# Kernel optimization log

Hardware: AMD Instinct MI355X
Metric: run time of the kernel (lower is better)

The kernel has to match this reference:

```python
import jax, jax.numpy as jnp
import numpy as np

B, S, D, H, F, L = 16, 512, 512, 8, 2048, 3  # L layers: 1 in blocks_1 + 2 in blocks_2
DK = D // H
EPS = 1e-5

def setup_inputs():
    key = jax.random.key(0)
    ks = jax.random.split(key, 10)
    sc = 1.0 / np.sqrt(D)
    return dict(
        q_embed_data=jax.random.normal(ks[0], (B, S, D), jnp.float32),
        qa_embed_data=jax.random.normal(ks[1], (B, S, D), jnp.float32),
        Wk=jax.random.normal(ks[2], (L, D, D), jnp.float32) * sc,
        bk=jnp.zeros((L, D), jnp.float32),
        Wv=jax.random.normal(ks[3], (L, D, D), jnp.float32) * sc,
        bv=jnp.zeros((L, D), jnp.float32),
        Wo=jax.random.normal(ks[4], (L, D, D), jnp.float32) * sc,
        bo=jnp.zeros((L, D), jnp.float32),
        gammas=jax.random.normal(ks[5], (L, H, 1, 1), jnp.float32) * 0.5,
        ln1_g=jnp.ones((L, D), jnp.float32),
        ln1_b=jnp.zeros((L, D), jnp.float32),
        W1=jax.random.normal(ks[6], (L, D, F), jnp.float32) * sc,
        b1=jnp.zeros((L, F), jnp.float32),
        W2=jax.random.normal(ks[7], (L, F, D), jnp.float32) * (1.0 / np.sqrt(F)),
        b2=jnp.zeros((L, D), jnp.float32),
        ln2_g=jnp.ones((L, D), jnp.float32),
        ln2_b=jnp.zeros((L, D), jnp.float32),
    )

def _ln(x, g, b):
    m = jnp.mean(x, -1, keepdims=True)
    v = jnp.mean((x - m) ** 2, -1, keepdims=True)
    return (x - m) * jax.lax.rsqrt(v + EPS) * g + b

def _attention(q, k, v, mask, gamma):
    # q,k,v: [B,H,S,DK]; mask: [1,1,S,S] bool; gamma: [H,1,1]
    scores = jnp.einsum('bhid,bhjd->bhij', q, k) / np.sqrt(DK)
    maskf = mask.astype(scores.dtype)
    # first (no-grad in torch) softmax pass for distance decay
    p = jax.nn.softmax(jnp.where(mask, scores, -1e32), axis=-1) * maskf
    distcum = jnp.cumsum(p, axis=-1)
    disttot = jnp.sum(p, axis=-1, keepdims=True)
    idx = jnp.arange(scores.shape[-1])
    pos = jnp.abs(idx[None, :] - idx[:, None]).astype(scores.dtype)[None, None]
    dist = jax.lax.stop_gradient(
        jnp.sqrt(jnp.clip((disttot - distcum) * pos, 0.0, None)))
    g = -jax.nn.softplus(gamma)[None]  # [1,H,1,1]
    total_effect = jnp.clip(jnp.exp(dist * g), 1e-5, 1e5)
    scores = jnp.where(mask, scores * total_effect, -1e32)
    attn = jax.nn.softmax(scores, axis=-1)
    return jnp.einsum('bhij,bhjd->bhid', attn, v)

def _mha(q_in, k_in, v_in, mask, Wk, bk, Wv, bv, Wo, bo, gamma):
    bsz = q_in.shape[0]
    def proj(x, W, b):
        return (x @ W + b).reshape(bsz, -1, H, DK).transpose(0, 2, 1, 3)
    q = proj(q_in, Wk, bk)  # kq_same=True -> q uses k_linear
    k = proj(k_in, Wk, bk)
    v = proj(v_in, Wv, bv)
    o = _attention(q, k, v, mask, gamma)
    o = o.transpose(0, 2, 1, 3).reshape(bsz, -1, D)
    return o @ Wo + bo

def _block(i, mask, query, key, values, apply_pos, P):
    q2 = _mha(query, key, values, mask, P['Wk'][i], P['bk'][i], P['Wv'][i],
              P['bv'][i], P['Wo'][i], P['bo'][i], P['gammas'][i])
    x = _ln(query + q2, P['ln1_g'][i], P['ln1_b'][i])
    if apply_pos:
        h = jax.nn.relu(x @ P['W1'][i] + P['b1'][i]) @ P['W2'][i] + P['b2'][i]
        x = _ln(x + h, P['ln2_g'][i], P['ln2_b'][i])
    return x

def reference(q_embed_data, qa_embed_data, Wk, bk, Wv, bv, Wo, bo, gammas,
              ln1_g, ln1_b, W1, b1, W2, b2, ln2_g, ln2_b):
    P = dict(Wk=Wk, bk=bk, Wv=Wv, bv=bv, Wo=Wo, bo=bo, gammas=gammas,
             ln1_g=ln1_g, ln1_b=ln1_b, W1=W1, b1=b1, W2=W2, b2=b2,
             ln2_g=ln2_g, ln2_b=ln2_b)
    s = q_embed_data.shape[1]
    mask1 = jnp.tril(jnp.ones((s, s), bool))[None, None]        # mask==1: current+past
    mask0 = jnp.tril(jnp.ones((s, s), bool), -1)[None, None]    # mask==0: strictly past
    y = qa_embed_data
    x = q_embed_data
    y = _block(0, mask1, y, y, y, True, P)    # blocks_1: knowledge encoder
    x = _block(1, mask1, x, x, x, False, P)   # blocks_2: question encoder (no FFN)
    x = _block(2, mask0, x, x, y, True, P)    # blocks_2: knowledge retriever
    return x
```

## Files before the change

### kernel.cpp

```cpp
#include <hip/hip_runtime.h>
#include <hip/hip_bf16.h>

#define Bdim 16
#define Sdim 512
#define Ddim 512
#define Hdim 8
#define DKdim 64
#define Fdim 2048
#define Mrows (Bdim * Sdim)

typedef __attribute__((ext_vector_type(8))) short  frag16;
typedef __attribute__((ext_vector_type(4))) float  f32x4;
typedef __attribute__((ext_vector_type(8))) unsigned short ushort8;
typedef __attribute__((ext_vector_type(4))) unsigned short ushort4v;

#if defined(__has_builtin)
#  if __has_builtin(__builtin_amdgcn_exp2f)
#    define EXP2(x) __builtin_amdgcn_exp2f(x)
#  endif
#endif
#ifndef EXP2
#  define EXP2(x) __expf((x) * 0.6931471805599453f)
#endif
#define SC2 0.18033688011112042f

__device__ __forceinline__ unsigned short f2b(float x) {
    union { float f; unsigned int u; } v; v.f = x;
    unsigned int r = (v.u + 0x7FFFu + ((v.u >> 16) & 1u)) >> 16;
    return (unsigned short)r;
}

__global__ __launch_bounds__(256) void gemm_mfma(
    const __hip_bfloat16* __restrict__ A, const __hip_bfloat16* __restrict__ Bt,
    const float* __restrict__ bias, const float* __restrict__ R,
    float* __restrict__ Cf, unsigned short* __restrict__ Cb,
    int M, int N, int K, int do_relu)
{
    __shared__ short As[2][128 * 32];
    __shared__ short Bs[2][128 * 32];

    const int t = threadIdx.x;
    const int lane = t & 63;
    const int wave = t >> 6;

    const int gx = gridDim.x;
    const int nb = gx * gridDim.y;
    const int lid = blockIdx.x + gx * blockIdx.y;
    const int wid = (lid & 7) * (nb >> 3) + (lid >> 3);
    const int bm = (wid / gx) * 128;
    const int bn = (wid % gx) * 128;

    const int wm = (wave >> 1) * 64;
    const int wn = (wave & 1) * 64;

    f32x4 acc[4][4] = {};
    const int lrow = lane >> 2;
    const int lcol = (lane & 3) * 8;

    auto stage = [&](int k0, int buf) {
#pragma unroll
        for (int i = 0; i < 2; ++i) {
            const int chunk = wave * 2 + i;
            const int row = chunk * 16 + lrow;
            const __hip_bfloat16* ga = A + (size_t)(bm + row) * K + k0 + lcol;
            const __hip_bfloat16* gb = Bt + (size_t)(bn + row) * K + k0 + lcol;
            __builtin_amdgcn_global_load_lds(
                (const __attribute__((address_space(1))) unsigned int*)ga,
                (__attribute__((address_space(3))) unsigned int*)(&As[buf][chunk * 512]),
                16, 0, 0);
            __builtin_amdgcn_global_load_lds(
                (const __attribute__((address_space(1))) unsigned int*)gb,
                (__attribute__((address_space(3))) unsigned int*)(&Bs[buf][chunk * 512]),
                16, 0, 0);
        }
    };

    const int fr = lane & 15;
    const int quad = lane >> 4;
    const int nk = K >> 5;

    stage(0, 0);
    __syncthreads();

    for (int it = 0; it < nk; ++it) {
        const int buf = it & 1;
        if (it + 1 < nk) stage((it + 1) << 5, buf ^ 1);
        frag16 af[4], bfr[4];
#pragma unroll
        for (int i = 0; i < 4; ++i) {
            af[i]  = *(const frag16*)(&As[buf][(wm + i * 16 + fr) * 32 + quad * 8]);
            bfr[i] = *(const frag16*)(&Bs[buf][(wn + i * 16 + fr) * 32 + quad * 8]);
        }
#pragma unroll
        for (int mi = 0; mi < 4; ++mi)
#pragma unroll
            for (int ni = 0; ni < 4; ++ni)
                acc[mi][ni] = __builtin_amdgcn_mfma_f32_16x16x32_bf16(
                    af[mi], bfr[ni], acc[mi][ni], 0, 0, 0);
        __syncthreads();
    }

#pragma unroll
    for (int mi = 0; mi < 4; ++mi) {
#pragma unroll
        for (int r = 0; r < 4; ++r) {
            const int m = bm + wm + mi * 16 + quad * 4 + r;
#pragma unroll
            for (int ni = 0; ni < 4; ++ni) {
                const int n = bn + wn + ni * 16 + fr;
                float v = acc[mi][ni][r] + bias[n];
                if (R) v += R[(size_t)m * N + n];
                if (do_relu) v = fmaxf(v, 0.f);
                if (Cf) Cf[(size_t)m * N + n] = v;
                if (Cb) Cb[(size_t)m * N + n] = f2b(v);
            }
        }
    }
}

__global__ __launch_bounds__(256) void gemm_n64(
    const unsigned short* __restrict__ A0, const unsigned short* __restrict__ A1,
    const unsigned short* __restrict__ B0, const unsigned short* __restrict__ B1,
    const float* __restrict__ bias0, const float* __restrict__ bias1,
    const float* __restrict__ R, float* __restrict__ Cf,
    unsigned short* __restrict__ Cb, unsigned short* __restrict__ CbT,
    int K)
{
    const int NN = 512;
    __shared__ short As[2][128 * 64];
    __shared__ short Bs[2][64 * 64];

    const int trans = blockIdx.z;
    const unsigned short* A  = trans ? A1 : A0;
    const unsigned short* Bt = trans ? B1 : B0;
    const float* bias        = trans ? bias1 : bias0;

    const int t = threadIdx.x;
    const int lane = t & 63;
    const int wave = t >> 6;

    const int lid = blockIdx.x + 8 * blockIdx.y;
    const int wid = (lid & 7) * 64 + (lid >> 3);
    const int bm = (wid >> 3) * 128;
    const int bn = (wid & 7) * 64;

    const int wm = (wave >> 1) * 64;
    const int wn = (wave & 1) * 32;

    f32x4 acc[4][2] = {};

    const int srcslot = (((lane & 7) ^ (lane >> 3)) << 3);
    const int rsub = lane >> 3;

    auto stage = [&](int k0, int buf) {
#pragma unroll
        for (int i = 0; i < 4; ++i) {
            const int row = i * 32 + wave * 8 + rsub;
            const unsigned short* ga = A + (size_t)(bm + row) * K + k0 + srcslot;
            __builtin_amdgcn_global_load_lds(
                (const __attribute__((address_space(1))) unsigned int*)ga,
                (__attribute__((address_space(3))) unsigned int*)(&As[buf][(i * 256 + wave * 64) * 8]),
                16, 0, 0);
        }
#pragma unroll
        for (int i = 0; i < 2; ++i) {
            const int row = i * 32 + wave * 8 + rsub;
            const unsigned short* gb = Bt + (size_t)(bn + row) * K + k0 + srcslot;
            __builtin_amdgcn_global_load_lds(
                (const __attribute__((address_space(1))) unsigned int*)gb,
                (__attribute__((address_space(3))) unsigned int*)(&Bs[buf][(i * 256 + wave * 64) * 8]),
                16, 0, 0);
        }
    };

    const int fr = lane & 15;
    const int quad = lane >> 4;
    const int sw = (fr & 7) << 3;
    const int nk = K >> 6;

    stage(0, 0);
    __syncthreads();

    for (int it = 0; it < nk; ++it) {
        const int buf = it & 1;
        if (it + 1 < nk) stage((it + 1) << 6, buf ^ 1);
        frag16 af[2][4], bfr[2][2];
#pragma unroll
        for (int ks = 0; ks < 2; ++ks) {
            const int col = (ks * 32 + quad * 8) ^ sw;
#pragma unroll
            for (int i = 0; i < 4; ++i)
                af[ks][i] = *(const frag16*)(&As[buf][(wm + i * 16 + fr) * 64 + col]);
#pragma unroll
            for (int i = 0; i < 2; ++i)
                bfr[ks][i] = *(const frag16*)(&Bs[buf][(wn + i * 16 + fr) * 64 + col]);
        }
#pragma unroll
        for (int ks = 0; ks < 2; ++ks)
#pragma unroll
            for (int mi = 0; mi < 4; ++mi)
#pragma unroll
                for (int ni = 0; ni < 2; ++ni)
                    acc[mi][ni] = __builtin_amdgcn_mfma_f32_16x16x32_bf16(
                        af[ks][mi], bfr[ks][ni], acc[mi][ni], 0, 0, 0);
        __syncthreads();
    }

    if (trans) {
#pragma unroll
        for (int mi = 0; mi < 4; ++mi)
#pragma unroll
            for (int ni = 0; ni < 2; ++ni) {
                const int m = bm + wm + mi * 16 + quad * 4;
                const int n = bn + wn + ni * 16 + fr;
                ushort4v o;
#pragma unroll
                for (int r = 0; r < 4; ++r) o[r] = f2b(acc[mi][ni][r] + bias[n]);
                const int bb = m >> 9, s = m & 511;
                const int hh = n >> 6, dd = n & 63;
                *(ushort4v*)(CbT + (((size_t)((bb * Hdim + hh) * DKdim + dd)) << 9) + s) = o;
            }
        return;
    }

#pragma unroll
    for (int mi = 0; mi < 4; ++mi) {
#pragma unroll
        for (int r = 0; r < 4; ++r) {
            const int m = bm + wm + mi * 16 + quad * 4 + r;
#pragma unroll
            for (int ni = 0; ni < 2; ++ni) {
                const int n = bn + wn + ni * 16 + fr;
                float v = acc[mi][ni][r] + bias[n];
                if (R) v += R[(size_t)m * NN + n];
                if (Cf) Cf[(size_t)m * NN + n] = v;
                if (Cb) Cb[(size_t)m * NN + n] = f2b(v);
            }
        }
    }
}

__global__ __launch_bounds__(256) void gemm_ffn2(
    const unsigned short* __restrict__ A, const unsigned short* __restrict__ Bt,
    const float* __restrict__ bias, const float* __restrict__ R,
    float* __restrict__ C0, float* __restrict__ C1)
{
    const int K = 2048, KH = 1024;
    __shared__ short As[2][128 * 64];
    __shared__ short Bs[2][64 * 64];

    const int z = blockIdx.z;
    const int kbase = z * KH;

    const int t = threadIdx.x;
    const int lane = t & 63;
    const int wave = t >> 6;

    const int lid = blockIdx.x + 8 * blockIdx.y;
    const int wid = (lid & 7) * 64 + (lid >> 3);
    const int bm = (wid >> 3) * 128;
    const int bn = (wid & 7) * 64;

    const int wm = (wave >> 1) * 64;
    const int wn = (wave & 1) * 32;

    f32x4 acc[4][2] = {};
    const int srcslot = (((lane & 7) ^ (lane >> 3)) << 3);
    const int rsub = lane >> 3;

    auto stage = [&](int k0, int buf) {
#pragma unroll
        for (int i = 0; i < 4; ++i) {
            const int row = i * 32 + wave * 8 + rsub;
            const unsigned short* ga = A + (size_t)(bm + row) * K + k0 + srcslot;
            __builtin_amdgcn_global_load_lds(
                (const __attribute__((address_space(1))) unsigned int*)ga,
                (__attribute__((address_space(3))) unsigned int*)(&As[buf][(i * 256 + wave * 64) * 8]),
                16, 0, 0);
        }
#pragma unroll
        for (int i = 0; i < 2; ++i) {
            const int row = i * 32 + wave * 8 + rsub;
            const unsigned short* gb = Bt + (size_t)(bn + row) * K + k0 + srcslot;
            __builtin_amdgcn_global_load_lds(
                (const __attribute__((address_space(1))) unsigned int*)gb,
                (__attribute__((address_space(3))) unsigned int*)(&Bs[buf][(i * 256 + wave * 64) * 8]),
                16, 0, 0);
        }
    };

    const int fr = lane & 15;
    const int quad = lane >> 4;
    const int sw = (fr & 7) << 3;
    const int nk = KH >> 6;

    stage(kbase, 0);
    __syncthreads();

    for (int it = 0; it < nk; ++it) {
        const int buf = it & 1;
        if (it + 1 < nk) stage(kbase + ((it + 1) << 6), buf ^ 1);
        frag16 af[2][4], bfr[2][2];
#pragma unroll
        for (int ks = 0; ks < 2; ++ks) {
            const int col = (ks * 32 + quad * 8) ^ sw;
#pragma unroll
            for (int i = 0; i < 4; ++i)
                af[ks][i] = *(const frag16*)(&As[buf][(wm + i * 16 + fr) * 64 + col]);
#pragma unroll
            for (int i = 0; i < 2; ++i)
                bfr[ks][i] = *(const frag16*)(&Bs[buf][(wn + i * 16 + fr) * 64 + col]);
        }
#pragma unroll
        for (int ks = 0; ks < 2; ++ks)
#pragma unroll
            for (int mi = 0; mi < 4; ++mi)
#pragma unroll
                for (int ni = 0; ni < 2; ++ni)
                    acc[mi][ni] = __builtin_amdgcn_mfma_f32_16x16x32_bf16(
                        af[ks][mi], bfr[ks][ni], acc[mi][ni], 0, 0, 0);
        __syncthreads();
    }

#pragma unroll
    for (int mi = 0; mi < 4; ++mi) {
#pragma unroll
        for (int r = 0; r < 4; ++r) {
            const int m = bm + wm + mi * 16 + quad * 4 + r;
#pragma unroll
            for (int ni = 0; ni < 2; ++ni) {
                const int n = bn + wn + ni * 16 + fr;
                if (z == 0)
                    C0[(size_t)m * 512 + n] = acc[mi][ni][r] + bias[n] + R[(size_t)m * 512 + n];
                else
                    C1[(size_t)m * 512 + n] = acc[mi][ni][r];
            }
        }
    }
}

__global__ __launch_bounds__(256) void gemm_kv4(
    const unsigned short* __restrict__ Ya, const unsigned short* __restrict__ Xa,
    const unsigned short* __restrict__ BtK0, const unsigned short* __restrict__ BtV0,
    const unsigned short* __restrict__ BtK1, const unsigned short* __restrict__ BtV1,
    const float* __restrict__ bk0, const float* __restrict__ bv0,
    const float* __restrict__ bk1, const float* __restrict__ bv1,
    unsigned short* __restrict__ K0, unsigned short* __restrict__ V0t,
    unsigned short* __restrict__ K1, unsigned short* __restrict__ V1t)
{
    const int K = 512;
    __shared__ short As[2][128 * 64];
    __shared__ short Bs[2][64 * 64];

    const int z = blockIdx.z;
    const unsigned short* A  = (z < 2) ? Ya : Xa;
    const unsigned short* Bt = (z == 0) ? BtK0 : (z == 1) ? BtV0 : (z == 2) ? BtK1 : BtV1;
    const float* bias        = (z == 0) ? bk0 : (z == 1) ? bv0 : (z == 2) ? bk1 : bv1;
    const int trans = z & 1;

    const int t = threadIdx.x;
    const int lane = t & 63;
    const int wave = t >> 6;

    const int lid = blockIdx.x + 8 * blockIdx.y;
    const int wid = (lid & 7) * 64 + (lid >> 3);
    const int bm = (wid >> 3) * 128;
    const int bn = (wid & 7) * 64;

    const int wm = (wave >> 1) * 64;
    const int wn = (wave & 1) * 32;

    f32x4 acc[4][2] = {};
    const int srcslot = (((lane & 7) ^ (lane >> 3)) << 3);
    const int rsub = lane >> 3;

    auto stage = [&](int k0, int buf) {
#pragma unroll
        for (int i = 0; i < 4; ++i) {
            const int row = i * 32 + wave * 8 + rsub;
            const unsigned short* ga = A + (size_t)(bm + row) * K + k0 + srcslot;
            __builtin_amdgcn_global_load_lds(
                (const __attribute__((address_space(1))) unsigned int*)ga,
                (__attribute__((address_space(3))) unsigned int*)(&As[buf][(i * 256 + wave * 64) * 8]),
                16, 0, 0);
        }
#pragma unroll
        for (int i = 0; i < 2; ++i) {
            const int row = i * 32 + wave * 8 + rsub;
            const unsigned short* gb = Bt + (size_t)(bn + row) * K + k0 + srcslot;
            __builtin_amdgcn_global_load_lds(
                (const __attribute__((address_space(1))) unsigned int*)gb,
                (__attribute__((address_space(3))) unsigned int*)(&Bs[buf][(i * 256 + wave * 64) * 8]),
                16, 0, 0);
        }
    };

    const int fr = lane & 15;
    const int quad = lane >> 4;
    const int sw = (fr & 7) << 3;
    const int nk = K >> 6;

    stage(0, 0);
    __syncthreads();

    for (int it = 0; it < nk; ++it) {
        const int buf = it & 1;
        if (it + 1 < nk) stage((it + 1) << 6, buf ^ 1);
        frag16 af[2][4], bfr[2][2];
#pragma unroll
        for (int ks = 0; ks < 2; ++ks) {
            const int col = (ks * 32 + quad * 8) ^ sw;
#pragma unroll
            for (int i = 0; i < 4; ++i)
                af[ks][i] = *(const frag16*)(&As[buf][(wm + i * 16 + fr) * 64 + col]);
#pragma unroll
            for (int i = 0; i < 2; ++i)
                bfr[ks][i] = *(const frag16*)(&Bs[buf][(wn + i * 16 + fr) * 64 + col]);
        }
#pragma unroll
        for (int ks = 0; ks < 2; ++ks)
#pragma unroll
            for (int mi = 0; mi < 4; ++mi)
#pragma unroll
                for (int ni = 0; ni < 2; ++ni)
                    acc[mi][ni] = __builtin_amdgcn_mfma_f32_16x16x32_bf16(
                        af[ks][mi], bfr[ks][ni], acc[mi][ni], 0, 0, 0);
        __syncthreads();
    }

    if (trans) {
        unsigned short* CbT = (z == 1) ? V0t : V1t;
#pragma unroll
        for (int mi = 0; mi < 4; ++mi)
#pragma unroll
            for (int ni = 0; ni < 2; ++ni) {
                const int m = bm + wm + mi * 16 + quad * 4;
                const int n = bn + wn + ni * 16 + fr;
                ushort4v o;
#pragma unroll
                for (int r = 0; r < 4; ++r) o[r] = f2b(acc[mi][ni][r] + bias[n]);
                const int bb = m >> 9, s = m & 511;
                const int hh = n >> 6, dd = n & 63;
                *(ushort4v*)(CbT + (((size_t)((bb * Hdim + hh) * DKdim + dd)) << 9) + s) = o;
            }
    } else {
        unsigned short* Cb = (z == 0) ? K0 : K1;
#pragma unroll
        for (int mi = 0; mi < 4; ++mi)
#pragma unroll
            for (int r = 0; r < 4; ++r) {
                const int m = bm + wm + mi * 16 + quad * 4 + r;
#pragma unroll
                for (int ni = 0; ni < 2; ++ni) {
                    const int n = bn + wn + ni * 16 + fr;
                    Cb[(size_t)m * 512 + n] = f2b(acc[mi][ni][r] + bias[n]);
                }
            }
    }
}

__global__ __launch_bounds__(256) void gemm_o2(
    const unsigned short* __restrict__ A0, const unsigned short* __restrict__ A1,
    const unsigned short* __restrict__ B0, const unsigned short* __restrict__ B1,
    const float* __restrict__ bias0, const float* __restrict__ bias1,
    const float* __restrict__ R0, const float* __restrict__ R1,
    float* __restrict__ C0, float* __restrict__ C1)
{
    const int K = 512;
    __shared__ short As[2][128 * 64];
    __shared__ short Bs[2][64 * 64];

    const int z = blockIdx.z;
    const unsigned short* A  = z ? A1 : A0;
    const unsigned short* Bt = z ? B1 : B0;
    const float* bias        = z ? bias1 : bias0;
    const float* R           = z ? R1 : R0;
    float* Cf                = z ? C1 : C0;

    const int t = threadIdx.x;
    const int lane = t & 63;
    const int wave = t >> 6;

    const int lid = blockIdx.x + 8 * blockIdx.y;
    const int wid = (lid & 7) * 64 + (lid >> 3);
    const int bm = (wid >> 3) * 128;
    const int bn = (wid & 7) * 64;

    const int wm = (wave >> 1) * 64;
    const int wn = (wave & 1) * 32;

    f32x4 acc[4][2] = {};
    const int srcslot = (((lane & 7) ^ (lane >> 3)) << 3);
    const int rsub = lane >> 3;

    auto stage = [&](int k0, int buf) {
#pragma unroll
        for (int i = 0; i < 4; ++i) {
            const int row = i * 32 + wave * 8 + rsub;
            const unsigned short* ga = A + (size_t)(bm + row) * K + k0 + srcslot;
            __builtin_amdgcn_global_load_lds(
                (const __attribute__((address_space(1))) unsigned int*)ga,
                (__attribute__((address_space(3))) unsigned int*)(&As[buf][(i * 256 + wave * 64) * 8]),
                16, 0, 0);
        }
#pragma unroll
        for (int i = 0; i < 2; ++i) {
            const int row = i * 32 + wave * 8 + rsub;
            const unsigned short* gb = Bt + (size_t)(bn + row) * K + k0 + srcslot;
            __builtin_amdgcn_global_load_lds(
                (const __attribute__((address_space(1))) unsigned int*)gb,
                (__attribute__((address_space(3))) unsigned int*)(&Bs[buf][(i * 256 + wave * 64) * 8]),
                16, 0, 0);
        }
    };

    const int fr = lane & 15;
    const int quad = lane >> 4;
    const int sw = (fr & 7) << 3;
    const int nk = K >> 6;

    stage(0, 0);
    __syncthreads();

    for (int it = 0; it < nk; ++it) {
        const int buf = it & 1;
        if (it + 1 < nk) stage((it + 1) << 6, buf ^ 1);
        frag16 af[2][4], bfr[2][2];
#pragma unroll
        for (int ks = 0; ks < 2; ++ks) {
            const int col = (ks * 32 + quad * 8) ^ sw;
#pragma unroll
            for (int i = 0; i < 4; ++i)
                af[ks][i] = *(const frag16*)(&As[buf][(wm + i * 16 + fr) * 64 + col]);
#pragma unroll
            for (int i = 0; i < 2; ++i)
                bfr[ks][i] = *(const frag16*)(&Bs[buf][(wn + i * 16 + fr) * 64 + col]);
        }
#pragma unroll
        for (int ks = 0; ks < 2; ++ks)
#pragma unroll
            for (int mi = 0; mi < 4; ++mi)
#pragma unroll
                for (int ni = 0; ni < 2; ++ni)
                    acc[mi][ni] = __builtin_amdgcn_mfma_f32_16x16x32_bf16(
                        af[ks][mi], bfr[ks][ni], acc[mi][ni], 0, 0, 0);
        __syncthreads();
    }

#pragma unroll
    for (int mi = 0; mi < 4; ++mi) {
#pragma unroll
        for (int r = 0; r < 4; ++r) {
            const int m = bm + wm + mi * 16 + quad * 4 + r;
#pragma unroll
            for (int ni = 0; ni < 2; ++ni) {
                const int n = bn + wn + ni * 16 + fr;
                Cf[(size_t)m * 512 + n] = acc[mi][ni][r] + bias[n] + R[(size_t)m * 512 + n];
            }
        }
    }
}

__global__ __launch_bounds__(256) void conv_b2(
    const float* __restrict__ X0, unsigned short* __restrict__ Y0,
    const float* __restrict__ X1, unsigned short* __restrict__ Y1,
    int halfBlocks)
{
    const int bid = blockIdx.x;
    const float* X = (bid < halfBlocks) ? X0 : X1;
    unsigned short* Y = (bid < halfBlocks) ? Y0 : Y1;
    const int lb = (bid < halfBlocks) ? bid : bid - halfBlocks;
    const size_t i = ((size_t)lb * 256 + threadIdx.x) * 8;
    float4 a = *(const float4*)(X + i);
    float4 b = *(const float4*)(X + i + 4);
    ushort8 o;
    o[0] = f2b(a.x); o[1] = f2b(a.y); o[2] = f2b(a.z); o[3] = f2b(a.w);
    o[4] = f2b(b.x); o[5] = f2b(b.y); o[6] = f2b(b.z); o[7] = f2b(b.w);
    *(ushort8*)(Y + i) = o;
}

__global__ __launch_bounds__(256) void wtrans_all(
    const float* __restrict__ Wk, const float* __restrict__ Wv,
    const float* __restrict__ Wo, const float* __restrict__ W1,
    const float* __restrict__ W2, unsigned short* __restrict__ dst)
{
    const int bid = blockIdx.x;
    const float* src; unsigned short* d; int K, N, tk, tn;
    if (bid < 576) {
        const int mat = bid >> 6, tile = bid & 63;
        const int l = mat / 3, wch = mat % 3;
        const float* W = (wch == 0) ? Wk : (wch == 1) ? Wv : Wo;
        src = W + (size_t)l * 262144;
        d = dst + (size_t)mat * 262144;
        K = 512; N = 512; tn = tile & 7; tk = tile >> 3;
    } else if (bid < 1088) {
        const int idx = bid - 576, l2 = idx >> 8, tile = idx & 255;
        src = W1 + (size_t)(l2 * 2) * (512 * 2048);
        d = dst + 9 * 262144 + (size_t)l2 * (512 * 2048);
        K = 512; N = 2048; tn = tile & 31; tk = tile >> 5;
    } else {
        const int idx = bid - 1088, l2 = idx >> 8, tile = idx & 255;
        src = W2 + (size_t)(l2 * 2) * (2048 * 512);
        d = dst + 9 * 262144 + 2 * (512 * 2048) + (size_t)l2 * (2048 * 512);
        K = 2048; N = 512; tn = tile & 7; tk = tile >> 3;
    }
    const int n0 = tn * 64, k0 = tk * 64;
    __shared__ float T[64][65];
    const int t = threadIdx.x;
    const int kl = t >> 4, n4 = (t & 15) << 2;
#pragma unroll
    for (int it = 0; it < 4; ++it) {
        const int k = kl + it * 16;
        float4 v = *(const float4*)(src + (size_t)(k0 + k) * N + n0 + n4);
        T[n4 + 0][k] = v.x; T[n4 + 1][k] = v.y;
        T[n4 + 2][k] = v.z; T[n4 + 3][k] = v.w;
    }
    __syncthreads();
    const int nl = t >> 3, k8 = (t & 7) << 3;
#pragma unroll
    for (int it = 0; it < 2; ++it) {
        const int n = nl + it * 32;
        ushort8 o;
#pragma unroll
        for (int c = 0; c < 8; ++c) o[c] = f2b(T[n][k8 + c]);
        *(ushort8*)(d + (size_t)(n0 + n) * K + k0 + k8) = o;
    }
}

__global__ __launch_bounds__(256, 8) void attn_flash8(
    const unsigned short* __restrict__ Kb0, const unsigned short* __restrict__ Vt0,
    const unsigned short* __restrict__ Kb1, const unsigned short* __restrict__ Vt1,
    const float* __restrict__ gam,
    unsigned short* __restrict__ Ob0, unsigned short* __restrict__ Ob1,
    int mask_type, int dual)
{
    __shared__ float CTw[16 * 33];
    __shared__ unsigned short Pst[4][16 * 36];
    __shared__ float S1s[4][16];
    __shared__ float S2s[4][16];
    __shared__ float OaccA[16 * 66];
    __shared__ float OaccB[16 * 66];

    int bh, layer;
    if (dual) { layer = blockIdx.x & 1; bh = blockIdx.x >> 1; }
    else      { layer = 0;              bh = blockIdx.x; }
    const unsigned short* Kb = layer ? Kb1 : Kb0;
    const unsigned short* Vt = layer ? Vt1 : Vt0;
    unsigned short* Ob       = layer ? Ob1 : Ob0;
    const float* g           = gam + layer * Hdim;

    const int h = bh & 7, b = bh >> 3;
    const int rk = blockIdx.y;
    const int tile = mask_type ? (31 - rk) : (rk == 0 ? 0 : 32 - rk);

    const int t = threadIdx.x, lane = t & 63, w = t >> 6;
    const int quad = lane >> 4, fr = lane & 15;
    const int q0 = tile * 16;
    const int iRow = q0 + fr;

    const unsigned short* kbase = Kb + (size_t)b * Sdim * Ddim + h * DKdim;
    const unsigned short* vtb = Vt + (size_t)(b * Hdim + h) * DKdim * Sdim;
    const float gneg2 = -log1pf(__expf(g[h])) * 1.4426950408889634f;

    frag16 aq0 = *(const frag16*)(kbase + (size_t)(q0 + fr) * Ddim + quad * 8);
    frag16 aq1 = *(const frag16*)(kbase + (size_t)(q0 + fr) * Ddim + 32 + quad * 8);

    float psum = 0.f;
    for (int jn = w; jn <= tile; jn += 4) {
        frag16 k0 = *(const frag16*)(kbase + (size_t)(jn * 16 + fr) * Ddim + quad * 8);
        frag16 k1 = *(const frag16*)(kbase + (size_t)(jn * 16 + fr) * Ddim + 32 + quad * 8);
        f32x4 z = {0.f, 0.f, 0.f, 0.f};
        z = __builtin_amdgcn_mfma_f32_16x16x32_bf16(k0, aq0, z, 0, 0, 0);
        z = __builtin_amdgcn_mfma_f32_16x16x32_bf16(k1, aq1, z, 0, 0, 0);
        float tq = 0.f;
        if (jn < tile) {
#pragma unroll
            for (int r = 0; r < 4; ++r) tq += EXP2(z[r] * SC2);
        } else {
#pragma unroll
            for (int r = 0; r < 4; ++r) {
                const bool valid = mask_type ? (quad * 4 + r <= fr)
                                             : (quad * 4 + r < fr);
                tq += valid ? EXP2(z[r] * SC2) : 0.f;
            }
        }
        psum += tq;
        float tt = tq;
        tt += __shfl_xor(tt, 16);
        tt += __shfl_xor(tt, 32);
        if (quad == 0) CTw[fr * 33 + jn] = tt;
    }
    {
        float s1 = psum;
        s1 += __shfl_xor(s1, 16);
        s1 += __shfl_xor(s1, 32);
        if (lane < 16) S1s[w][lane] = s1;
    }
    __syncthreads();

    if (w == 0 && lane < 16) {
        float run = 0.f;
        for (int jn = tile; jn >= 0; --jn) {
            const float tv = CTw[lane * 33 + jn];
            CTw[lane * 33 + jn] = run;
            run += tv;
        }
    }
    __syncthreads();

    const float rsum1 = 1.f / (S1s[0][fr] + S1s[1][fr] + S1s[2][fr] + S1s[3][fr]);
    unsigned short* Pw = Pst[w];
    const bool fm_blk = (mask_type == 0) && (tile == 0);
    const bool fmrow = fm_blk && (fr == 0);
    const int umax = fm_blk ? (Sdim / 32 - 1) : (tile >> 1);
    float sum2p = 0.f;
    f32x4 oacc[4] = {};

    for (int u = umax - w; u >= 0; u -= 4) {
#pragma unroll
        for (int half = 0; half < 2; ++half) {
            const int jn = 2 * u + half;
            uint2 pku;
            if (jn > tile) {
                const unsigned int pv = fmrow ? 0x3F803F80u : 0u;
                pku.x = pv; pku.y = pv;
                sum2p += fmrow ? 4.f : 0.f;
            } else {
                frag16 k0 = *(const frag16*)(kbase + (size_t)(jn * 16 + fr) * Ddim + quad * 8);
                frag16 k1 = *(const frag16*)(kbase + (size_t)(jn * 16 + fr) * Ddim + 32 + quad * 8);
                f32x4 z = {0.f, 0.f, 0.f, 0.f};
                z = __builtin_amdgcn_mfma_f32_16x16x32_bf16(k0, aq0, z, 0, 0, 0);
                z = __builtin_amdgcn_mfma_f32_16x16x32_bf16(k1, aq1, z, 0, 0, 0);
                const bool full = (jn < tile);
                float s2r[4], lsuf[4];
                float tq = 0.f;
#pragma unroll
                for (int r = 3; r >= 0; --r) {
                    lsuf[r] = tq;
                    s2r[r] = z[r] * SC2;
                    float e1 = EXP2(s2r[r]);
                    if (!full) {
                        const bool valid = mask_type ? (quad * 4 + r <= fr)
                                                     : (quad * 4 + r < fr);
                        e1 = valid ? e1 : 0.f;
                    }
                    tq += e1;
                }
                float incl = tq;
                {
                    float u1 = __shfl_down(incl, 16);
                    incl += (quad < 3) ? u1 : 0.f;
                    float u2 = __shfl_down(incl, 32);
                    incl += (quad < 2) ? u2 : 0.f;
                }
                const float base = CTw[fr * 33 + jn] + (incl - tq);
                const float pos0 = (float)(iRow - (jn * 16 + quad * 4));
                float e2v[4];
#pragma unroll
                for (int r = 0; r < 4; ++r) {
                    const float ratio = (base + lsuf[r]) * rsum1;
                    const float arg = ratio * fabsf(pos0 - (float)r);
                    const float te = fmaxf(EXP2(gneg2 * sqrtf(arg)), 1e-5f);
                    float e2 = EXP2(s2r[r] * te);
                    if (!full) {
                        const bool valid = mask_type ? (quad * 4 + r <= fr)
                                                     : (quad * 4 + r < fr);
                        e2 = valid ? e2 : (fmrow ? 1.f : 0.f);
                    }
                    sum2p += e2;
                    e2v[r] = e2;
                }
                union { __hip_bfloat162 hh; unsigned int u; } c0, c1;
                c0.hh = __float22bfloat162_rn(make_float2(e2v[0], e2v[1]));
                c1.hh = __float22bfloat162_rn(make_float2(e2v[2], e2v[3]));
                pku.x = c0.u; pku.y = c1.u;
            }
            *(uint2*)(Pw + fr * 36 + half * 16 + quad * 4) = pku;
        }
        frag16 pf = *(const frag16*)(Pw + fr * 36 + quad * 8);
        const int jb = u * 32;
#pragma unroll
        for (int dt = 0; dt < 4; ++dt) {
            frag16 vf = *(const frag16*)(vtb + (size_t)(dt * 16 + fr) * Sdim + jb + quad * 8);
            oacc[dt] = __builtin_amdgcn_mfma_f32_16x16x32_bf16(pf, vf, oacc[dt], 0, 0, 0);
        }
    }

    {
        float s2 = sum2p;
        s2 += __shfl_xor(s2, 16);
        s2 += __shfl_xor(s2, 32);
        if (lane < 16) S2s[w][lane] = s2;
    }
    if (w == 1) {
#pragma unroll
        for (int dt = 0; dt < 4; ++dt)
#pragma unroll
            for (int r = 0; r < 4; ++r)
                OaccA[(quad * 4 + r) * 66 + dt * 16 + fr] = oacc[dt][r];
    }
    if (w == 3) {
#pragma unroll
        for (int dt = 0; dt < 4; ++dt)
#pragma unroll
            for (int r = 0; r < 4; ++r)
                OaccB[(quad * 4 + r) * 66 + dt * 16 + fr] = oacc[dt][r];
    }
    __syncthreads();
    if (w == 0) {
#pragma unroll
        for (int dt = 0; dt < 4; ++dt)
#pragma unroll
            for (int r = 0; r < 4; ++r)
                oacc[dt][r] += OaccA[(quad * 4 + r) * 66 + dt * 16 + fr];
    }
    if (w == 2) {
#pragma unroll
        for (int dt = 0; dt < 4; ++dt)
#pragma unroll
            for (int r = 0; r < 4; ++r)
                oacc[dt][r] += OaccB[(quad * 4 + r) * 66 + dt * 16 + fr];
    }
    __syncthreads();
    if (w == 2) {
#pragma unroll
        for (int dt = 0; dt < 4; ++dt)
#pragma unroll
            for (int r = 0; r < 4; ++r)
                OaccA[(quad * 4 + r) * 66 + dt * 16 + fr] = oacc[dt][r];
    }
    __syncthreads();

    if (w == 0) {
        const float rs2 = 1.f / (S2s[0][fr] + S2s[1][fr] + S2s[2][fr] + S2s[3][fr]);
        float rs2q[4];
#pragma unroll
        for (int r = 0; r < 4; ++r) rs2q[r] = __shfl(rs2, quad * 4 + r);

        unsigned short* obase = Ob + ((size_t)(b * Sdim + q0)) * Ddim + h * DKdim;
#pragma unroll
        for (int dt = 0; dt < 4; ++dt)
#pragma unroll
            for (int r = 0; r < 4; ++r) {
                const float v = oacc[dt][r] + OaccA[(quad * 4 + r) * 66 + dt * 16 + fr];
                obase[(size_t)(quad * 4 + r) * Ddim + dt * 16 + fr] = f2b(v * rs2q[r]);
            }
    }
}

__device__ __forceinline__ void ln_row_wave(
    const float* __restrict__ X, const float* __restrict__ P,
    const float* __restrict__ g, const float* __restrict__ bta,
    float* __restrict__ Y, unsigned short* __restrict__ Yb,
    int row, int lane)
{
    const size_t base = (size_t)row * Ddim + lane * 8;
    float4 a = *(const float4*)(X + base);
    float4 b = *(const float4*)(X + base + 4);
    if (P) {
        float4 pa = *(const float4*)(P + base);
        float4 pb = *(const float4*)(P + base + 4);
        a.x += pa.x; a.y += pa.y; a.z += pa.z; a.w += pa.w;
        b.x += pb.x; b.y += pb.y; b.z += pb.z; b.w += pb.w;
    }
    float s  = a.x + a.y + a.z + a.w + b.x + b.y + b.z + b.w;
    float s2 = a.x * a.x + a.y * a.y + a.z * a.z + a.w * a.w
             + b.x * b.x + b.y * b.y + b.z * b.z + b.w * b.w;
#pragma unroll
    for (int off = 1; off < 64; off <<= 1) {
        s  += __shfl_xor(s, off);
        s2 += __shfl_xor(s2, off);
    }
    const float mean = s * (1.f / Ddim);
    const float var = s2 * (1.f / Ddim) - mean * mean;
    const float rs = rsqrtf(var + 1e-5f);
    float4 ga = *(const float4*)(g + lane * 8);
    float4 gb = *(const float4*)(g + lane * 8 + 4);
    float4 ba = *(const float4*)(bta + lane * 8);
    float4 bb = *(const float4*)(bta + lane * 8 + 4);
    float y[8];
    y[0] = (a.x - mean) * rs * ga.x + ba.x;
    y[1] = (a.y - mean) * rs * ga.y + ba.y;
    y[2] = (a.z - mean) * rs * ga.z + ba.z;
    y[3] = (a.w - mean) * rs * ga.w + ba.w;
    y[4] = (b.x - mean) * rs * gb.x + bb.x;
    y[5] = (b.y - mean) * rs * gb.y + bb.y;
    y[6] = (b.z - mean) * rs * gb.z + bb.z;
    y[7] = (b.w - mean) * rs * gb.w + bb.w;
    if (Y) {
        *(float4*)(Y + base)     = make_float4(y[0], y[1], y[2], y[3]);
        *(float4*)(Y + base + 4) = make_float4(y[4], y[5], y[6], y[7]);
    }
    if (Yb) {
        ushort8 o;
#pragma unroll
        for (int c = 0; c < 8; ++c) o[c] = f2b(y[c]);
        *(ushort8*)(Yb + base) = o;
    }
}

__global__ __launch_bounds__(256) void ln_w1(
    const float* __restrict__ X, const float* __restrict__ P,
    const float* __restrict__ g, const float* __restrict__ bta,
    float* __restrict__ Y, unsigned short* __restrict__ Yb)
{
    const int row = blockIdx.x * 4 + (threadIdx.x >> 6);
    ln_row_wave(X, P, g, bta, Y, Yb, row, threadIdx.x & 63);
}

__global__ __launch_bounds__(256) void ln_w2(
    const float* __restrict__ Xa, const float* __restrict__ ga,
    const float* __restrict__ ba, float* __restrict__ Ya,
    unsigned short* __restrict__ Yba,
    const float* __restrict__ Xb, const float* __restrict__ gb,
    const float* __restrict__ bb, float* __restrict__ Yb2,
    unsigned short* __restrict__ Ybb)
{
    const int row = blockIdx.x * 4 + (threadIdx.x >> 6);
    if (row < Mrows)
        ln_row_wave(Xa, nullptr, ga, ba, Ya, Yba, row, threadIdx.x & 63);
    else
        ln_row_wave(Xb, nullptr, gb, bb, Yb2, Ybb, row - Mrows, threadIdx.x & 63);
}

extern "C" void kernel_launch(void* const* d_in, const int* in_sizes, int n_in,
                              void* d_out, int out_size, void* d_ws, size_t ws_size,
                              hipStream_t stream)
{
    const float* x0     = (const float*)d_in[0];
    const float* y0     = (const float*)d_in[1];
    const float* Wk     = (const float*)d_in[2];
    const float* bk     = (const float*)d_in[3];
    const float* Wv     = (const float*)d_in[4];
    const float* bv     = (const float*)d_in[5];
    const float* Wo     = (const float*)d_in[6];
    const float* bo     = (const float*)d_in[7];
    const float* gammas = (const float*)d_in[8];
    const float* ln1g   = (const float*)d_in[9];
    const float* ln1b   = (const float*)d_in[10];
    const float* W1     = (const float*)d_in[11];
    const float* b1     = (const float*)d_in[12];
    const float* W2     = (const float*)d_in[13];
    const float* b2     = (const float*)d_in[14];
    const float* ln2g   = (const float*)d_in[15];
    const float* ln2b   = (const float*)d_in[16];

    const size_t NBSD = (size_t)Mrows * Ddim;
    float* ws = (float*)d_ws;
    float* T1   = ws;
    float* X1   = T1 + NBSD;
    float* Xbuf = X1 + NBSD;
    unsigned short* Kbf = (unsigned short*)(Xbuf + NBSD);
    unsigned short* Vt  = Kbf + NBSD;
    unsigned short* AOb = Vt + NBSD;
    unsigned short* Abf = AOb + NBSD;
    unsigned short* Xbf = Abf + NBSD;
    unsigned short* Ybf = Xbf + NBSD;
    unsigned short* Hbb = Ybf + NBSD;
    unsigned short* WtAll = Hbb + (size_t)Mrows * Fdim;

    unsigned short* Xb_in = Hbb;
    unsigned short* AOb1  = Hbb + NBSD;
    unsigned short* Yb_in = Hbb + 2 * NBSD;
    unsigned short* Kbf1  = Abf;
    unsigned short* Vt1   = Ybf;
    float* T1b = (float*)d_out;
    float* P1  = (float*)AOb;

    auto WtK = [&](int l) { return WtAll + (size_t)(l * 3 + 0) * 262144; };
    auto WtV = [&](int l) { return WtAll + (size_t)(l * 3 + 1) * 262144; };
    auto WtO = [&](int l) { return WtAll + (size_t)(l * 3 + 2) * 262144; };
    auto Wt1 = [&](int l) { return WtAll + 9 * 262144 + (size_t)(l >> 1) * (512 * 2048); };
    auto Wt2 = [&](int l) { return WtAll + 9 * 262144 + 2 * (512 * 2048) + (size_t)(l >> 1) * (2048 * 512); };

    const int convBlocks = (int)(NBSD / 2048);

    wtrans_all<<<1600, 256, 0, stream>>>(Wk, Wv, Wo, W1, W2, WtAll);
    conv_b2<<<2 * convBlocks, 256, 0, stream>>>(y0, Yb_in, x0, Xb_in, convBlocks);
    gemm_kv4<<<dim3(8, 64, 4), 256, 0, stream>>>(
        Yb_in, Xb_in, WtK(0), WtV(0), WtK(1), WtV(1),
        bk, bv, bk + Ddim, bv + Ddim,
        Kbf, Vt, Kbf1, Vt1);
    attn_flash8<<<dim3(2 * Bdim * Hdim, Sdim / 16, 1), 256, 0, stream>>>(
        Kbf, Vt, Kbf1, Vt1, gammas, AOb, AOb1, 1, 1);
    gemm_o2<<<dim3(8, 64, 2), 256, 0, stream>>>(
        AOb, AOb1, WtO(0), WtO(1), bo, bo + Ddim, y0, x0, T1, T1b);
    ln_w2<<<2 * Mrows / 4, 256, 0, stream>>>(
        T1, ln1g, ln1b, X1, Abf,
        T1b, ln1g + Ddim, ln1b + Ddim, Xbuf, Xbf);
    gemm_mfma<<<dim3(Fdim / 128, Mrows / 128), 256, 0, stream>>>(
        (const __hip_bfloat16*)Abf, (const __hip_bfloat16*)Wt1(0),
        b1, nullptr, nullptr, Hbb, Mrows, Fdim, Ddim, 1);
    gemm_ffn2<<<dim3(8, 64, 2), 256, 0, stream>>>(
        Hbb, Wt2(0), b2, X1, T1, P1);
    ln_w1<<<Mrows / 4, 256, 0, stream>>>(T1, P1, ln2g, ln2b, nullptr, Ybf);

    const int l = 2;
    gemm_n64<<<dim3(8, 64, 2), 256, 0, stream>>>(
        Xbf, Ybf, WtK(l), WtV(l), bk + l * Ddim, bv + l * Ddim,
        nullptr, nullptr, Kbf, Vt, Ddim);
    attn_flash8<<<dim3(Bdim * Hdim, Sdim / 16, 1), 256, 0, stream>>>(
        Kbf, Vt, Kbf, Vt, gammas + (size_t)l * Hdim, AOb, AOb, 0, 0);
    gemm_n64<<<dim3(8, 64, 1), 256, 0, stream>>>(
        AOb, AOb, WtO(l), WtO(l), bo + l * Ddim, bo + l * Ddim,
        Xbuf, T1, nullptr, nullptr, Ddim);
    ln_w1<<<Mrows / 4, 256, 0, stream>>>(T1, nullptr,
        ln1g + (size_t)l * Ddim, ln1b + (size_t)l * Ddim, X1, Abf);
    gemm_mfma<<<dim3(Fdim / 128, Mrows / 128), 256, 0, stream>>>(
        (const __hip_bfloat16*)Abf, (const __hip_bfloat16*)Wt1(l),
        b1 + (size_t)l * Fdim, nullptr, nullptr, Hbb, Mrows, Fdim, Ddim, 1);
    gemm_ffn2<<<dim3(8, 64, 2), 256, 0, stream>>>(
        Hbb, Wt2(l), b2 + (size_t)l * Ddim, X1, T1, P1);
    ln_w1<<<Mrows / 4, 256, 0, stream>>>(T1, P1,
        ln2g + (size_t)l * Ddim, ln2b + (size_t)l * Ddim, (float*)d_out, nullptr);
}
```

Before: 562.4 us.

## Split-K the output projections and use 32-bit offsets in attention

Generalizes the FFN2 split-K kernel to take K as a parameter and applies it to the layer-2 output projection. gemm_o2 is now split in half along K over four z-slices, with the second half's partial sums folded in by the LayerNorm kernels. The goal is more blocks per launch for these short-K GEMMs, at the cost of extra fp32 partial-buffer traffic. The attention kernel switches to precomputed 32-bit unsigned offsets and computes sqrt as x*rsqrt to trim address and ALU work. gemm_o2's partial buffers alias X1 and Xbuf, which are read and written in place by ln_w2.

```diff
diff --git a/kernel.cpp b/kernel.cpp
--- a/kernel.cpp
+++ b/kernel.cpp
@@ -240,17 +240,17 @@
     }
 }
 
-__global__ __launch_bounds__(256) void gemm_ffn2(
+__global__ __launch_bounds__(256) void gemm_splitk(
     const unsigned short* __restrict__ A, const unsigned short* __restrict__ Bt,
     const float* __restrict__ bias, const float* __restrict__ R,
-    float* __restrict__ C0, float* __restrict__ C1)
-{
-    const int K = 2048, KH = 1024;
+    float* __restrict__ C0, float* __restrict__ C1,
+    int K, int KH)
+{
     __shared__ short As[2][128 * 64];
     __shared__ short Bs[2][64 * 64];
 
     const int z = blockIdx.z;
-    const int kbase = z * KH;
+    const int kb0 = z * KH;
 
     const int t = threadIdx.x;
     const int lane = t & 63;
@@ -294,12 +294,12 @@
     const int sw = (fr & 7) << 3;
     const int nk = KH >> 6;
 
-    stage(kbase, 0);
+    stage(kb0, 0);
     __syncthreads();
 
     for (int it = 0; it < nk; ++it) {
         const int buf = it & 1;
-        if (it + 1 < nk) stage(kbase + ((it + 1) << 6), buf ^ 1);
+        if (it + 1 < nk) stage(kb0 + ((it + 1) << 6), buf ^ 1);
         frag16 af[2][4], bfr[2][2];
 #pragma unroll
         for (int ks = 0; ks < 2; ++ks) {
@@ -464,18 +464,20 @@
     const unsigned short* __restrict__ B0, const unsigned short* __restrict__ B1,
     const float* __restrict__ bias0, const float* __restrict__ bias1,
     const float* __restrict__ R0, const float* __restrict__ R1,
-    float* __restrict__ C0, float* __restrict__ C1)
-{
-    const int K = 512;
+    float* __restrict__ C0, float* __restrict__ C1,
+    float* __restrict__ P0, float* __restrict__ P1)
+{
+    const int K = 512, KH = 256;
     __shared__ short As[2][128 * 64];
     __shared__ short Bs[2][64 * 64];
 
-    const int z = blockIdx.z;
-    const unsigned short* A  = z ? A1 : A0;
-    const unsigned short* Bt = z ? B1 : B0;
-    const float* bias        = z ? bias1 : bias0;
-    const float* R           = z ? R1 : R0;
-    float* Cf                = z ? C1 : C0;
+    const int zl = blockIdx.z >> 1, kh = blockIdx.z & 1;
+    const unsigned short* A  = zl ? A1 : A0;
+    const unsigned short* Bt = zl ? B1 : B0;
+    const float* bias        = zl ? bias1 : bias0;
+    const float* R           = zl ? R1 : R0;
+    float* Cf                = kh ? (zl ? P1 : P0) : (zl ? C1 : C0);
+    const int kb0 = kh * KH;
 
     const int t = threadIdx.x;
     const int lane = t & 63;
@@ -517,14 +519,14 @@
     const int fr = lane & 15;
     const int quad = lane >> 4;
     const int sw = (fr & 7) << 3;
-    const int nk = K >> 6;
-
-    stage(0, 0);
+    const int nk = KH >> 6;
+
+    stage(kb0, 0);
     __syncthreads();
 
     for (int it = 0; it < nk; ++it) {
         const int buf = it & 1;
-        if (it + 1 < nk) stage((it + 1) << 6, buf ^ 1);
+        if (it + 1 < nk) stage(kb0 + ((it + 1) << 6), buf ^ 1);
         frag16 af[2][4], bfr[2][2];
 #pragma unroll
         for (int ks = 0; ks < 2; ++ks) {
@@ -555,7 +557,9 @@
 #pragma unroll
             for (int ni = 0; ni < 2; ++ni) {
                 const int n = bn + wn + ni * 16 + fr;
-                Cf[(size_t)m * 512 + n] = acc[mi][ni][r] + bias[n] + R[(size_t)m * 512 + n];
+                float v = acc[mi][ni][r];
+                if (kh == 0) v += bias[n] + R[(size_t)m * 512 + n];
+                Cf[(size_t)m * 512 + n] = v;
             }
         }
     }
@@ -627,7 +631,7 @@
     }
 }
 
-__global__ __launch_bounds__(256, 8) void attn_flash8(
+__global__ __launch_bounds__(256, 8) void attn_flash9(
     const unsigned short* __restrict__ Kb0, const unsigned short* __restrict__ Vt0,
     const unsigned short* __restrict__ Kb1, const unsigned short* __restrict__ Vt1,
     const float* __restrict__ gam,
@@ -662,33 +666,39 @@
     const unsigned short* vtb = Vt + (size_t)(b * Hdim + h) * DKdim * Sdim;
     const float gneg2 = -log1pf(__expf(g[h])) * 1.4426950408889634f;
 
-    frag16 aq0 = *(const frag16*)(kbase + (size_t)(q0 + fr) * Ddim + quad * 8);
-    frag16 aq1 = *(const frag16*)(kbase + (size_t)(q0 + fr) * Ddim + 32 + quad * 8);
+    const unsigned lane_off = ((unsigned)fr << 9) + (unsigned)quad * 8;
+    const unsigned kvstep = 16u * Ddim;
+
+    frag16 aq0 = *(const frag16*)(kbase + ((unsigned)q0 << 9) + lane_off);
+    frag16 aq1 = *(const frag16*)(kbase + ((unsigned)q0 << 9) + lane_off + 32);
 
     float psum = 0.f;
-    for (int jn = w; jn <= tile; jn += 4) {
-        frag16 k0 = *(const frag16*)(kbase + (size_t)(jn * 16 + fr) * Ddim + quad * 8);
-        frag16 k1 = *(const frag16*)(kbase + (size_t)(jn * 16 + fr) * Ddim + 32 + quad * 8);
-        f32x4 z = {0.f, 0.f, 0.f, 0.f};
-        z = __builtin_amdgcn_mfma_f32_16x16x32_bf16(k0, aq0, z, 0, 0, 0);
-        z = __builtin_amdgcn_mfma_f32_16x16x32_bf16(k1, aq1, z, 0, 0, 0);
-        float tq = 0.f;
-        if (jn < tile) {
-#pragma unroll
-            for (int r = 0; r < 4; ++r) tq += EXP2(z[r] * SC2);
-        } else {
-#pragma unroll
-            for (int r = 0; r < 4; ++r) {
-                const bool valid = mask_type ? (quad * 4 + r <= fr)
-                                             : (quad * 4 + r < fr);
-                tq += valid ? EXP2(z[r] * SC2) : 0.f;
+    {
+        unsigned ko = (unsigned)w * kvstep + lane_off;
+        for (int jn = w; jn <= tile; jn += 4, ko += 4 * kvstep) {
+            frag16 k0 = *(const frag16*)(kbase + ko);
+            frag16 k1 = *(const frag16*)(kbase + ko + 32);
+            f32x4 z = {0.f, 0.f, 0.f, 0.f};
+            z = __builtin_amdgcn_mfma_f32_16x16x32_bf16(k0, aq0, z, 0, 0, 0);
+            z = __builtin_amdgcn_mfma_f32_16x16x32_bf16(k1, aq1, z, 0, 0, 0);
+            float tq = 0.f;
+            if (jn < tile) {
+#pragma unroll
+                for (int r = 0; r < 4; ++r) tq += EXP2(z[r] * SC2);
+            } else {
+#pragma unroll
+                for (int r = 0; r < 4; ++r) {
+                    const bool valid = mask_type ? (quad * 4 + r <= fr)
+                                                 : (quad * 4 + r < fr);
+                    tq += valid ? EXP2(z[r] * SC2) : 0.f;
+                }
             }
-        }
-        psum += tq;
-        float tt = tq;
-        tt += __shfl_xor(tt, 16);
-        tt += __shfl_xor(tt, 32);
-        if (quad == 0) CTw[fr * 33 + jn] = tt;
+            psum += tq;
+            float tt = tq;
+            tt += __shfl_xor(tt, 16);
+            tt += __shfl_xor(tt, 32);
+            if (quad == 0) CTw[fr * 33 + jn] = tt;
+        }
     }
     {
         float s1 = psum;
@@ -717,6 +727,7 @@
     f32x4 oacc[4] = {};
 
     for (int u = umax - w; u >= 0; u -= 4) {
+        const unsigned ko2 = ((unsigned)u << 14) + lane_off;
 #pragma unroll
         for (int half = 0; half < 2; ++half) {
             const int jn = 2 * u + half;
@@ -726,8 +737,9 @@
                 pku.x = pv; pku.y = pv;
                 sum2p += fmrow ? 4.f : 0.f;
             } else {
-                frag16 k0 = *(const frag16*)(kbase + (size_t)(jn * 16 + fr) * Ddim + quad * 8);
-                frag16 k1 = *(const frag16*)(kbase + (size_t)(jn * 16 + fr) * Ddim + 32 + quad * 8);
+                const unsigned koh = ko2 + (unsigned)half * kvstep;
+                frag16 k0 = *(const frag16*)(kbase + koh);
+                frag16 k1 = *(const frag16*)(kbase + koh + 32);
                 f32x4 z = {0.f, 0.f, 0.f, 0.f};
                 z = __builtin_amdgcn_mfma_f32_16x16x32_bf16(k0, aq0, z, 0, 0, 0);
                 z = __builtin_amdgcn_mfma_f32_16x16x32_bf16(k1, aq1, z, 0, 0, 0);
@@ -760,7 +772,8 @@
                 for (int r = 0; r < 4; ++r) {
                     const float ratio = (base + lsuf[r]) * rsum1;
                     const float arg = ratio * fabsf(pos0 - (float)r);
-                    const float te = fmaxf(EXP2(gneg2 * sqrtf(arg)), 1e-5f);
+                    const float sq = arg * rsqrtf(fmaxf(arg, 1e-30f));
+                    const float te = fmaxf(EXP2(gneg2 * sq), 1e-5f);
                     float e2 = EXP2(s2r[r] * te);
                     if (!full) {
                         const bool valid = mask_type ? (quad * 4 + r <= fr)
@@ -778,10 +791,10 @@
             *(uint2*)(Pw + fr * 36 + half * 16 + quad * 4) = pku;
         }
         frag16 pf = *(const frag16*)(Pw + fr * 36 + quad * 8);
-        const int jb = u * 32;
+        const unsigned vo = lane_off + ((unsigned)u << 5);
 #pragma unroll
         for (int dt = 0; dt < 4; ++dt) {
-            frag16 vf = *(const frag16*)(vtb + (size_t)(dt * 16 + fr) * Sdim + jb + quad * 8);
+            frag16 vf = *(const frag16*)(vtb + vo + (unsigned)dt * 8192u);
             oacc[dt] = __builtin_amdgcn_mfma_f32_16x16x32_bf16(pf, vf, oacc[dt], 0, 0, 0);
         }
     }
@@ -909,18 +922,18 @@
 }
 
 __global__ __launch_bounds__(256) void ln_w2(
-    const float* __restrict__ Xa, const float* __restrict__ ga,
-    const float* __restrict__ ba, float* __restrict__ Ya,
-    unsigned short* __restrict__ Yba,
-    const float* __restrict__ Xb, const float* __restrict__ gb,
-    const float* __restrict__ bb, float* __restrict__ Yb2,
-    unsigned short* __restrict__ Ybb)
+    const float* __restrict__ Xa, const float* __restrict__ Pa,
+    const float* __restrict__ ga, const float* __restrict__ ba,
+    float* __restrict__ Ya, unsigned short* __restrict__ Yba,
+    const float* __restrict__ Xb, const float* __restrict__ Pb,
+    const float* __restrict__ gb, const float* __restrict__ bb,
+    float* __restrict__ Yb2, unsigned short* __restrict__ Ybb)
 {
     const int row = blockIdx.x * 4 + (threadIdx.x >> 6);
     if (row < Mrows)
-        ln_row_wave(Xa, nullptr, ga, ba, Ya, Yba, row, threadIdx.x & 63);
+        ln_row_wave(Xa, Pa, ga, ba, Ya, Yba, row, threadIdx.x & 63);
     else
-        ln_row_wave(Xb, nullptr, gb, bb, Yb2, Ybb, row - Mrows, threadIdx.x & 63);
+        ln_row_wave(Xb, Pb, gb, bb, Yb2, Ybb, row - Mrows, threadIdx.x & 63);
 }
 
 extern "C" void kernel_launch(void* const* d_in, const int* in_sizes, int n_in,
@@ -966,6 +979,7 @@
     unsigned short* Vt1   = Ybf;
     float* T1b = (float*)d_out;
     float* P1  = (float*)AOb;
+    float* PO2 = (float*)Hbb;
 
     auto WtK = [&](int l) { return WtAll + (size_t)(l * 3 + 0) * 262144; };
     auto WtV = [&](int l) { return WtAll + (size_t)(l * 3 + 1) * 262144; };
@@ -981,36 +995,36 @@
         Yb_in, Xb_in, WtK(0), WtV(0), WtK(1), WtV(1),
         bk, bv, bk + Ddim, bv + Ddim,
         Kbf, Vt, Kbf1, Vt1);
-    attn_flash8<<<dim3(2 * Bdim * Hdim, Sdim / 16, 1), 256, 0, stream>>>(
+    attn_flash9<<<dim3(2 * Bdim * Hdim, Sdim / 16, 1), 256, 0, stream>>>(
         Kbf, Vt, Kbf1, Vt1, gammas, AOb, AOb1, 1, 1);
-    gemm_o2<<<dim3(8, 64, 2), 256, 0, stream>>>(
-        AOb, AOb1, WtO(0), WtO(1), bo, bo + Ddim, y0, x0, T1, T1b);
+    gemm_o2<<<dim3(8, 64, 4), 256, 0, stream>>>(
+        AOb, AOb1, WtO(0), WtO(1), bo, bo + Ddim, y0, x0,
+        T1, T1b, X1 , Xbuf );
     ln_w2<<<2 * Mrows / 4, 256, 0, stream>>>(
-        T1, ln1g, ln1b, X1, Abf,
-        T1b, ln1g + Ddim, ln1b + Ddim, Xbuf, Xbf);
+        T1, X1, ln1g, ln1b, X1, Abf,
+        T1b, Xbuf, ln1g + Ddim, ln1b + Ddim, Xbuf, Xbf);
     gemm_mfma<<<dim3(Fdim / 128, Mrows / 128), 256, 0, stream>>>(
         (const __hip_bfloat16*)Abf, (const __hip_bfloat16*)Wt1(0),
         b1, nullptr, nullptr, Hbb, Mrows, Fdim, Ddim, 1);
-    gemm_ffn2<<<dim3(8, 64, 2), 256, 0, stream>>>(
-        Hbb, Wt2(0), b2, X1, T1, P1);
+    gemm_splitk<<<dim3(8, 64, 2), 256, 0, stream>>>(
+        Hbb, Wt2(0), b2, X1, T1, P1, 2048, 1024);
     ln_w1<<<Mrows / 4, 256, 0, stream>>>(T1, P1, ln2g, ln2b, nullptr, Ybf);
 
     const int l = 2;
     gemm_n64<<<dim3(8, 64, 2), 256, 0, stream>>>(
         Xbf, Ybf, WtK(l), WtV(l), bk + l * Ddim, bv + l * Ddim,
         nullptr, nullptr, Kbf, Vt, Ddim);
-    attn_flash8<<<dim3(Bdim * Hdim, Sdim / 16, 1), 256, 0, stream>>>(
+    attn_flash9<<<dim3(Bdim * Hdim, Sdim / 16, 1), 256, 0, stream>>>(
         Kbf, Vt, Kbf, Vt, gammas + (size_t)l * Hdim, AOb, AOb, 0, 0);
-    gemm_n64<<<dim3(8, 64, 1), 256, 0, stream>>>(
-        AOb, AOb, WtO(l), WtO(l), bo + l * Ddim, bo + l * Ddim,
-        Xbuf, T1, nullptr, nullptr, Ddim);
-    ln_w1<<<Mrows / 4, 256, 0, stream>>>(T1, nullptr,
+    gemm_splitk<<<dim3(8, 64, 2), 256, 0, stream>>>(
+        AOb, WtO(l), bo + l * Ddim, Xbuf, T1, PO2, 512, 256);
+    ln_w1<<<Mrows / 4, 256, 0, stream>>>(T1, PO2,
         ln1g + (size_t)l * Ddim, ln1b + (size_t)l * Ddim, X1, Abf);
     gemm_mfma<<<dim3(Fdim / 128, Mrows / 128), 256, 0, stream>>>(
         (const __hip_bfloat16*)Abf, (const __hip_bfloat16*)Wt1(l),
         b1 + (size_t)l * Fdim, nullptr, nullptr, Hbb, Mrows, Fdim, Ddim, 1);
-    gemm_ffn2<<<dim3(8, 64, 2), 256, 0, stream>>>(
-        Hbb, Wt2(l), b2 + (size_t)l * Ddim, X1, T1, P1);
+    gemm_splitk<<<dim3(8, 64, 2), 256, 0, stream>>>(
+        Hbb, Wt2(l), b2 + (size_t)l * Ddim, X1, T1, P1, 2048, 1024);
     ln_w1<<<Mrows / 4, 256, 0, stream>>>(T1, P1,
         ln2g + (size_t)l * Ddim, ln2b + (size_t)l * Ddim, (float*)d_out, nullptr);
 }
```

Measured after the change: 569.8 us. Within noise of the previous version (+1.3%).
